# Kernel optimization log

Measured on AMD Instinct MI355X. Metric: run time of the kernel, lower is better.

Reference implementation:

```python
import jax, jax.numpy as jnp
import numpy as np

B, N = 32, 8192
NUM_CLASSES = 40
SA1_DIMS = (3, 64, 64, 128)      # grouped relative xyz only (in_channels=3 -> no extra features)
SA2_DIMS = (131, 128, 128, 256)  # 128 SA1 features + 3 relative xyz
LOC_DIMS = (256, 256, 512, 1024)
GLOB_DIMS = (1024, 512, 256)


def _fps(xyz, m):
    """Farthest point sampling. xyz: [B,N,3] -> indices [B,m] (first index is point 0)."""
    b, n, _ = xyz.shape
    big = jnp.asarray(1e10, xyz.dtype)

    def step(carry, _):
        dists, last = carry                                   # [B,N], [B]
        p = jnp.take_along_axis(xyz, last[:, None, None], axis=1)  # [B,1,3]
        d = jnp.sum((xyz - p) ** 2, axis=-1)                  # [B,N]
        dists = jnp.minimum(dists, d)
        nxt = jnp.argmax(dists, axis=-1).astype(jnp.int32)
        return (dists, nxt), nxt

    init = (jnp.full((b, n), big, xyz.dtype), jnp.zeros((b,), jnp.int32))
    _, rest = jax.lax.scan(step, init, None, length=m - 1)    # [m-1,B]
    return jnp.concatenate([jnp.zeros((b, 1), jnp.int32), rest.T], axis=1)


def _ball_query(xyz, new_xyz, radius, k):
    """First-k points within radius of each centroid, padded with the first hit (CUDA ball_query semantics)."""
    d2 = jnp.sum((new_xyz[:, :, None, :] - xyz[:, None, :, :]) ** 2, axis=-1)  # [B,M,N]
    valid = d2 < radius * radius
    n = xyz.shape[1]
    ar = jnp.arange(n, dtype=jnp.int32)
    order_key = jnp.where(valid, ar, ar + n)                  # valid points sort first, in index order
    _, idx = jax.lax.top_k(-order_key, k)                     # [B,M,K] first-k valid indices
    num_valid = jnp.sum(valid, axis=-1)                       # [B,M]
    idx = jnp.where(jnp.arange(k) < num_valid[..., None], idx, idx[..., :1])
    return idx.astype(jnp.int32)


_gather = jax.vmap(lambda p, i: p[i])  # p:[N,C], i:[M,K] -> [M,K,C], vmapped over batch


def _sa(xyz, feats, m, radius, k, ws, bs):
    """PointNetSAModule: FPS -> ball query -> group (relative xyz [+feat]) -> SharedMLP -> max over K."""
    cidx = _fps(xyz, m)
    new_xyz = jnp.take_along_axis(xyz, cidx[:, :, None], axis=1)   # [B,m,3]
    idx = _ball_query(xyz, new_xyz, radius, k)                     # [B,m,k]
    x = _gather(xyz, idx) - new_xyz[:, :, None, :]                 # [B,m,k,3]
    if feats is not None:
        x = jnp.concatenate([x, _gather(feats, idx)], axis=-1)
    for w, b in zip(ws, bs):  # Conv2d(1x1)+BN(eval, folded)+ReLU
        x = jax.nn.relu(jnp.einsum('bmkc,oc->bmko', x, w) + b)
    return new_xyz, jnp.max(x, axis=2)                             # [B,m,C_out]


def _forward(points, sa1_w0, sa1_b0, sa1_w1, sa1_b1, sa1_w2, sa1_b2,
             sa2_w0, sa2_b0, sa2_w1, sa2_b1, sa2_w2, sa2_b2,
             loc_w0, loc_b0, loc_w1, loc_b1, loc_w2, loc_b2,
             glob_w0, glob_b0, glob_w1, glob_b1, cls_w, cls_b):
    xyz = jnp.transpose(points, (0, 2, 1))                         # [B,N,3]
    new_xyz, feats = _sa(xyz, None, 512, 0.2, 32,
                         (sa1_w0, sa1_w1, sa1_w2), (sa1_b0, sa1_b1, sa1_b2))
    _, feats = _sa(new_xyz, feats, 128, 0.4, 64,
                   (sa2_w0, sa2_w1, sa2_w2), (sa2_b0, sa2_b1, sa2_b2))
    x = feats                                                      # [B,128,256]
    for w, b in ((loc_w0, loc_b0), (loc_w1, loc_b1), (loc_w2, loc_b2)):
        x = jax.nn.relu(jnp.einsum('bnc,oc->bno', x, w) + b)       # SharedMLP (Conv1d+BN+ReLU)
    x = jnp.max(x, axis=1)                                         # global max-pool -> [B,1024]
    for w, b in ((glob_w0, glob_b0), (glob_w1, glob_b1)):          # MLP (dropout in eval = identity)
        x = jax.nn.relu(x @ w.T + b)
    return x @ cls_w.T + cls_b                                     # cls_logits [B,40]


def setup_inputs() -> dict:
    key = jax.random.key(0)
    ks = iter(jax.random.split(key, 64))
    inp = {}
    # unit-cube point cloud so radii 0.2/0.4 are geometrically meaningful
    inp['points'] = jax.random.uniform(next(ks), (B, 3, N), jnp.float32, -1.0, 1.0)

    def lin(co, ci):
        return jax.random.normal(next(ks), (co, ci), jnp.float32) / np.sqrt(ci)

    for name, dims in (('sa1', SA1_DIMS), ('sa2', SA2_DIMS), ('loc', LOC_DIMS)):
        for i in range(len(dims) - 1):
            inp[f'{name}_w{i}'] = lin(dims[i + 1], dims[i])
            inp[f'{name}_b{i}'] = 0.01 * jax.random.normal(next(ks), (dims[i + 1],), jnp.float32)
    for i in range(2):
        inp[f'glob_w{i}'] = lin(GLOB_DIMS[i + 1], GLOB_DIMS[i])
        inp[f'glob_b{i}'] = 0.01 * jax.random.normal(next(ks), (GLOB_DIMS[i + 1],), jnp.float32)
    inp['cls_w'] = lin(NUM_CLASSES, GLOB_DIMS[-1])
    inp['cls_b'] = jnp.zeros((NUM_CLASSES,), jnp.float32)
    return inp


def reference(points, sa1_w0, sa1_b0, sa1_w1, sa1_b1, sa1_w2, sa1_b2,
              sa2_w0, sa2_b0, sa2_w1, sa2_b1, sa2_w2, sa2_b2,
              loc_w0, loc_b0, loc_w1, loc_b1, loc_w2, loc_b2,
              glob_w0, glob_b0, glob_w1, glob_b1, cls_w, cls_b):
    return _forward(points, sa1_w0, sa1_b0, sa1_w1, sa1_b1, sa1_w2, sa1_b2,
                    sa2_w0, sa2_b0, sa2_w1, sa2_b1, sa2_w2, sa2_b2,
                    loc_w0, loc_b0, loc_w1, loc_b1, loc_w2, loc_b2,
                    glob_w0, glob_b0, glob_w1, glob_b1, cls_w, cls_b)
```

## Files before the change

### kernel.cpp

```cpp
#include <hip/hip_runtime.h>
#include <hip/hip_bf16.h>
#include <cstdint>

#define CDIV(a,b) (((a)+(b)-1)/(b))

typedef short s8v __attribute__((ext_vector_type(8)));
typedef float f4v __attribute__((ext_vector_type(4)));
typedef float f2v __attribute__((ext_vector_type(2)));

__device__ __forceinline__ unsigned short f2bf_bits(float v) {
  __hip_bfloat16 b = __float2bfloat16(v);
  unsigned short u; __builtin_memcpy(&u, &b, 2);
  return u;
}
__device__ __forceinline__ void bsplit(float v, unsigned short& h, unsigned short& l) {
  __hip_bfloat16 hb = __float2bfloat16(v);
  float hf = __bfloat162float(hb);
  unsigned short hu; __builtin_memcpy(&hu, &hb, 2);
  h = hu;
  l = f2bf_bits(v - hf);
}

__device__ __forceinline__ void gl2lds16(const void* g, void* l, int lane) {
#if __has_builtin(__builtin_amdgcn_global_load_lds)
  __builtin_amdgcn_global_load_lds(
      (const __attribute__((address_space(1))) unsigned int*)g,
      (__attribute__((address_space(3))) unsigned int*)l, 16, 0, 0);
#else
  ((uint4*)l)[lane] = *(const uint4*)g;
#endif
}

__device__ __forceinline__ void agpr_put(float& slot, float v) {
  asm volatile("v_accvgpr_write_b32 %0, %1" : "=a"(slot) : "v"(v));
}
__device__ __forceinline__ float agpr_get(const float& slot) {
  float v;
  asm volatile("v_accvgpr_read_b32 %0, %1" : "=v"(v) : "a"(slot));
  return v;
}

__device__ __forceinline__ f2v pk_add(f2v a, f2v b) {
  f2v d; asm("v_pk_add_f32 %0, %1, %2" : "=v"(d) : "v"(a), "v"(b)); return d;
}
__device__ __forceinline__ f2v pk_mul(f2v a, f2v b) {
  f2v d; asm("v_pk_mul_f32 %0, %1, %2" : "=v"(d) : "v"(a), "v"(b)); return d;
}
__device__ __forceinline__ f2v pk_fma(f2v a, f2v b, f2v c) {
  f2v d; asm("v_pk_fma_f32 %0, %1, %2, %3" : "=v"(d) : "v"(a), "v"(b), "v"(c)); return d;
}

template<int C>
__device__ __forceinline__ unsigned dpp32(unsigned v) {
  return (unsigned)__builtin_amdgcn_update_dpp((int)v, (int)v, C, 0xF, 0xF, false);
}
template<int C>
__device__ __forceinline__ unsigned long long red_key(unsigned long long pk) {
  unsigned lo = dpp32<C>((unsigned)pk);
  unsigned hi = dpp32<C>((unsigned)(pk >> 32));
  unsigned long long p2 = ((unsigned long long)hi << 32) | lo;
  return (p2 > pk) ? p2 : pk;
}

template<int NPTS, int MOUT, int NTHR>
__global__ __launch_bounds__(NTHR, 1) void fps_kernel(
    const float* __restrict__ pts, int bstride, int cstride,
    int* __restrict__ out_idx)
{
  constexpr int PPT = NPTS / NTHR;
  constexpr int NP2 = PPT / 2;
  constexpr int NW  = NTHR / 64;
  const int b = blockIdx.x, t = threadIdx.x;
  const int lane = t & 63;
  const int wid = t >> 6;
  const float* px = pts + (size_t)b * bstride;
  const float* py = px + cstride;
  const float* pz = px + 2 * cstride;
  __shared__ float s_x[NPTS], s_y[NPTS], s_z[NPTS];
  __shared__ unsigned long long s_key[2][NW];
  __shared__ int s_out[MOUT];

  float ax[PPT], ay[PPT], az[PPT];
  f2v dsv[NP2];
#pragma unroll
  for (int j = 0; j < PPT; ++j) {
    int i = t + j * NTHR;
    float x = px[i], y = py[i], z = pz[i];
    s_x[i] = x; s_y[i] = y; s_z[i] = z;
    agpr_put(ax[j], x); agpr_put(ay[j], y); agpr_put(az[j], z);
  }
#pragma unroll
  for (int q = 0; q < NP2; ++q) dsv[q] = (f2v){1e10f, 1e10f};
  if (t == 0) s_out[0] = 0;
  float lx = px[0], ly = py[0], lz = pz[0];
  __syncthreads();

  for (int it = 1; it < MOUT; ++it) {
    const f2v nlx = (f2v){-lx, -lx};
    const f2v nly = (f2v){-ly, -ly};
    const f2v nlz = (f2v){-lz, -lz};
    float bestv = -1.0f; int bestj = 0;
#pragma unroll
    for (int q = 0; q < NP2; ++q) {
      f2v x2, y2, z2;
      x2.x = agpr_get(ax[2 * q]); x2.y = agpr_get(ax[2 * q + 1]);
      y2.x = agpr_get(ay[2 * q]); y2.y = agpr_get(ay[2 * q + 1]);
      z2.x = agpr_get(az[2 * q]); z2.y = agpr_get(az[2 * q + 1]);
      f2v dx = pk_add(x2, nlx);
      f2v dy = pk_add(y2, nly);
      f2v dz = pk_add(z2, nlz);
      f2v d2 = pk_fma(dz, dz, pk_fma(dy, dy, pk_mul(dx, dx)));
      float nd0 = fminf(dsv[q].x, d2.x);
      float nd1 = fminf(dsv[q].y, d2.y);
      dsv[q].x = nd0; dsv[q].y = nd1;
      if (nd0 > bestv) { bestv = nd0; bestj = 2 * q; }
      if (nd1 > bestv) { bestv = nd1; bestj = 2 * q + 1; }
    }
    const int besti = t + bestj * NTHR;
    unsigned long long pk =
        ((unsigned long long)__float_as_uint(bestv) << 32) | (unsigned)(~(unsigned)besti);
    pk = red_key<0x111>(pk);
    pk = red_key<0x112>(pk);
    pk = red_key<0x114>(pk);
    pk = red_key<0x118>(pk);
    pk = red_key<0x142>(pk);
    pk = red_key<0x143>(pk);
    int widx;
    if constexpr (NW == 1) {
      widx = (int)(~(unsigned)__builtin_amdgcn_readlane((int)(unsigned)pk, 63));
    } else {
      const int pb = it & 1;
      if (lane == 63) s_key[pb][wid] = pk;
      __syncthreads();
      unsigned long long ck = s_key[pb][lane & (NW - 1)];
      if (NW >= 2) ck = red_key<0x111>(ck);
      if (NW >= 4) ck = red_key<0x112>(ck);
      if (NW >= 8) ck = red_key<0x114>(ck);
      widx = (int)(~(unsigned)__builtin_amdgcn_readlane((int)(unsigned)ck, NW - 1));
    }
    lx = s_x[widx]; ly = s_y[widx]; lz = s_z[widx];
    if (t == 0) s_out[it] = widx;
  }
  __syncthreads();
  for (int i = t; i < MOUT; i += NTHR)
    out_idx[(size_t)b * MOUT + i] = s_out[i];
}

__global__ void gatherc_kernel(
    const float* __restrict__ pts, int bstride, int cstride,
    const int* __restrict__ cidx, int M,
    float* __restrict__ aos, float* __restrict__ soa)
{
  const int b = blockIdx.x, t = threadIdx.x;
  const int i = cidx[(size_t)b * M + t];
  const float* p = pts + (size_t)b * bstride;
  float x = p[i], y = p[cstride + i], z = p[2 * cstride + i];
  size_t g = (size_t)b * M + t;
  aos[g * 3 + 0] = x; aos[g * 3 + 1] = y; aos[g * 3 + 2] = z;
  soa[(size_t)b * 3 * M + t]         = x;
  soa[(size_t)b * 3 * M + M + t]     = y;
  soa[(size_t)b * 3 * M + 2 * M + t] = z;
}

template<int NPTS, int KNB, int MC>
__global__ __launch_bounds__(64) void ballq_wave(
    const float* __restrict__ pts, int bstride, int cstride,
    const float* __restrict__ cents, int* __restrict__ out, float r2)
{
  constexpr int NCH = NPTS / 64;
  const int g = blockIdx.x;
  const int b = g / MC;
  const int lane = threadIdx.x;
  const float* px = pts + (size_t)b * bstride;
  const float* py = px + cstride;
  const float* pz = px + 2 * cstride;
  const float cx = cents[g * 3 + 0], cy = cents[g * 3 + 1], cz = cents[g * 3 + 2];
  __shared__ int s_idx[KNB];
  float nx = px[lane], ny = py[lane], nz = pz[lane];
  int base = 0;
  for (int c = 0; c < NCH; ++c) {
    float X = nx, Y = ny, Z = nz;
    if (c + 1 < NCH) {
      int i2 = (c + 1) * 64 + lane;
      nx = px[i2]; ny = py[i2]; nz = pz[i2];
    }
    float dx = X - cx, dy = Y - cy, dz = Z - cz;
    bool valid = (dx * dx + dy * dy + dz * dz) < r2;
    unsigned long long mask = __ballot(valid);
    int rank = __popcll(mask & ((1ull << lane) - 1ull));
    int pos = base + rank;
    if (valid && pos < KNB) s_idx[pos] = c * 64 + lane;
    base += __popcll(mask);
    if (base >= KNB) break;
  }
  int total = base < KNB ? base : KNB;
  int first = s_idx[0];
  if (lane < KNB)
    out[(size_t)g * KNB + lane] = (lane < total) ? s_idx[lane] : first;
}

__global__ __launch_bounds__(256, 1) void sa1_fused(
    const float* __restrict__ pts, const int* __restrict__ idx1,
    const float* __restrict__ cents,
    const float* __restrict__ w0, const float* __restrict__ b0,
    const unsigned short* __restrict__ w1h, const unsigned short* __restrict__ w1l,
    const float* __restrict__ b1,
    const unsigned short* __restrict__ w2h, const unsigned short* __restrict__ w2l,
    const float* __restrict__ b2,
    unsigned short* __restrict__ f1h, unsigned short* __restrict__ f1l)
{
  __shared__ __align__(16) unsigned short sY[2][128 * 72];
  __shared__ __align__(16) unsigned short sZ[2][128 * 72];
  __shared__ __align__(16) unsigned short sW[2][64 * 72];
  __shared__ float sw0[192];
  __shared__ float sb0[64];

  const int tid = threadIdx.x, lane = tid & 63, wid = tid >> 6;
  const int wm = wid & 1, wn = wid >> 1;
  const int mn15 = lane & 15, kgrp = lane >> 4;
  const int bk = blockIdx.x;

  if (tid < 192) sw0[tid] = w0[tid];
  else sb0[tid - 192] = b0[tid - 192];
  for (int gi = tid; gi < 1024; gi += 256) {
    const int pl = gi >> 9, idx = gi & 511;
    const int n = idx >> 3, k8 = idx & 7;
    const uint4 v = ((const uint4*)(pl ? w1l : w1h))[idx];
    *(uint4*)&sW[pl][n * 72 + k8 * 8] = v;
  }
  __syncthreads();

  {
    const int rl = tid >> 1, half = tid & 1;
    const int r = bk * 128 + rl;
    const int gl = r >> 5, j = r & 31, b = gl >> 9;
    const int i = idx1[(size_t)gl * 32 + j];
    const float* px = pts + (size_t)b * 24576;
    const float x = px[i]         - cents[gl * 3 + 0];
    const float y = px[8192 + i]  - cents[gl * 3 + 1];
    const float z = px[16384 + i] - cents[gl * 3 + 2];
    union { unsigned short us[32]; uint4 v[4]; } ph, pl4;
#pragma unroll
    for (int u = 0; u < 32; ++u) {
      const int o = half * 32 + u;
      float v = sw0[o * 3] * x + sw0[o * 3 + 1] * y + sw0[o * 3 + 2] * z + sb0[o];
      v = fmaxf(v, 0.f);
      bsplit(v, ph.us[u], pl4.us[u]);
    }
    const int base = rl * 72 + half * 32;
#pragma unroll
    for (int g = 0; g < 4; ++g) {
      *(uint4*)&sY[0][base + g * 8] = ph.v[g];
      *(uint4*)&sY[1][base + g * 8] = pl4.v[g];
    }
  }
  __syncthreads();

  {
    f4v acc[4][2];
#pragma unroll
    for (int a = 0; a < 4; ++a)
#pragma unroll
      for (int c = 0; c < 2; ++c) acc[a][c] = (f4v){0.f, 0.f, 0.f, 0.f};
#pragma unroll
    for (int kc = 0; kc < 2; ++kc) {
      const int k0 = kc * 32;
      s8v af[2][4], bf[2][2];
#pragma unroll
      for (int mt = 0; mt < 4; ++mt) {
        const int m = wm * 64 + mt * 16 + mn15;
        af[0][mt] = *(const s8v*)&sY[0][m * 72 + k0 + kgrp * 8];
        af[1][mt] = *(const s8v*)&sY[1][m * 72 + k0 + kgrp * 8];
      }
#pragma unroll
      for (int nt = 0; nt < 2; ++nt) {
        const int n = wn * 32 + nt * 16 + mn15;
        bf[0][nt] = *(const s8v*)&sW[0][n * 72 + k0 + kgrp * 8];
        bf[1][nt] = *(const s8v*)&sW[1][n * 72 + k0 + kgrp * 8];
      }
#pragma unroll
      for (int mt = 0; mt < 4; ++mt)
#pragma unroll
        for (int nt = 0; nt < 2; ++nt) {
          acc[mt][nt] = __builtin_amdgcn_mfma_f32_16x16x32_bf16(af[0][mt], bf[0][nt], acc[mt][nt], 0, 0, 0);
          acc[mt][nt] = __builtin_amdgcn_mfma_f32_16x16x32_bf16(af[0][mt], bf[1][nt], acc[mt][nt], 0, 0, 0);
          acc[mt][nt] = __builtin_amdgcn_mfma_f32_16x16x32_bf16(af[1][mt], bf[0][nt], acc[mt][nt], 0, 0, 0);
        }
    }
#pragma unroll
    for (int nt = 0; nt < 2; ++nt) {
      const int n = wn * 32 + nt * 16 + mn15;
      const float bv = b1[n];
#pragma unroll
      for (int mt = 0; mt < 4; ++mt)
#pragma unroll
        for (int r = 0; r < 4; ++r) {
          const int m = wm * 64 + mt * 16 + (lane >> 4) * 4 + r;
          float v = fmaxf(acc[mt][nt][r] + bv, 0.f);
          unsigned short h, l; bsplit(v, h, l);
          sZ[0][m * 72 + n] = h;
          sZ[1][m * 72 + n] = l;
        }
    }
  }
  __syncthreads();

  for (int gi = tid; gi < 2048; gi += 256) {
    const int pl = gi >> 10, idx = gi & 1023;
    const int n = idx >> 3, k8 = idx & 7;
    const uint4 v = ((const uint4*)(pl ? w2l : w2h))[idx];
    *(uint4*)&sY[pl][n * 72 + k8 * 8] = v;
  }
  __syncthreads();

  {
    f4v acc[4][4];
#pragma unroll
    for (int a = 0; a < 4; ++a)
#pragma unroll
      for (int c = 0; c < 4; ++c) acc[a][c] = (f4v){0.f, 0.f, 0.f, 0.f};
#pragma unroll
    for (int kc = 0; kc < 2; ++kc) {
      const int k0 = kc * 32;
      s8v af[2][4], bf[2][4];
#pragma unroll
      for (int mt = 0; mt < 4; ++mt) {
        const int m = wm * 64 + mt * 16 + mn15;
        af[0][mt] = *(const s8v*)&sZ[0][m * 72 + k0 + kgrp * 8];
        af[1][mt] = *(const s8v*)&sZ[1][m * 72 + k0 + kgrp * 8];
      }
#pragma unroll
      for (int nt = 0; nt < 4; ++nt) {
        const int n = wn * 64 + nt * 16 + mn15;
        bf[0][nt] = *(const s8v*)&sY[0][n * 72 + k0 + kgrp * 8];
        bf[1][nt] = *(const s8v*)&sY[1][n * 72 + k0 + kgrp * 8];
      }
#pragma unroll
      for (int mt = 0; mt < 4; ++mt)
#pragma unroll
        for (int nt = 0; nt < 4; ++nt) {
          acc[mt][nt] = __builtin_amdgcn_mfma_f32_16x16x32_bf16(af[0][mt], bf[0][nt], acc[mt][nt], 0, 0, 0);
          acc[mt][nt] = __builtin_amdgcn_mfma_f32_16x16x32_bf16(af[0][mt], bf[1][nt], acc[mt][nt], 0, 0, 0);
          acc[mt][nt] = __builtin_amdgcn_mfma_f32_16x16x32_bf16(af[1][mt], bf[0][nt], acc[mt][nt], 0, 0, 0);
        }
    }
#pragma unroll
    for (int gq = 0; gq < 2; ++gq)
#pragma unroll
      for (int nt = 0; nt < 4; ++nt) {
        const int n = wn * 64 + nt * 16 + mn15;
        float v = -1e30f;
#pragma unroll
        for (int mt = 2 * gq; mt < 2 * gq + 2; ++mt)
#pragma unroll
          for (int r = 0; r < 4; ++r) v = fmaxf(v, acc[mt][nt][r]);
        v = fmaxf(v + b2[n], 0.f);
        v = fmaxf(v, __shfl_xor(v, 16, 64));
        v = fmaxf(v, __shfl_xor(v, 32, 64));
        if (lane < 16) {
          const size_t row = (size_t)bk * 4 + wm * 2 + gq;
          unsigned short h, l; bsplit(v, h, l);
          f1h[row * 128 + n] = h;
          f1l[row * 128 + n] = l;
        }
      }
  }
}

__global__ void gather2p_kernel(
    const float* __restrict__ nx1_aos,
    const unsigned short* __restrict__ f1h, const unsigned short* __restrict__ f1l,
    const int* __restrict__ idx2, const float* __restrict__ nx2_aos,
    unsigned short* __restrict__ Xh, unsigned short* __restrict__ Xl, int g0)
{
  const int r = blockIdx.x * 4 + threadIdx.y;
  const int lane = threadIdx.x;
  int gl = r >> 6, j = r & 63;
  int gg = g0 + gl;
  int b  = gg >> 7;
  int i  = idx2[(size_t)gg * 64 + j];
  int p  = b * 512 + i;
  size_t ro = (size_t)r * 160;
  const int slot = lane & 31;
  const bool isL = lane >= 32;
  unsigned short* dst = isL ? Xl : Xh;
  const unsigned short* f1 = isL ? f1l : f1h;
  if (slot < 16) {
    ((uint4*)(dst + ro))[slot] = ((const uint4*)(f1 + (size_t)p * 128))[slot];
  } else if (slot == 16) {
    union { unsigned short us[8]; uint4 v; } pk;
#pragma unroll
    for (int u = 0; u < 8; ++u) pk.us[u] = 0;
#pragma unroll
    for (int c = 0; c < 3; ++c) {
      float v = nx1_aos[(size_t)p * 3 + c] - nx2_aos[(size_t)gg * 3 + c];
      unsigned short h, l; bsplit(v, h, l);
      pk.us[c] = isL ? l : h;
    }
    ((uint4*)(dst + ro))[16] = pk.v;
  } else if (slot <= 19) {
    ((uint4*)(dst + ro))[slot] = make_uint4(0, 0, 0, 0);
  }
}

struct WSplitArgs {
  const float* src[9];
  unsigned short* h[9];
  unsigned short* l[9];
  int K[9];
  int KP[9];
  int perm[9];
  int cum[10];
};
__global__ void wsplit_all(WSplitArgs a) {
  int i = blockIdx.x * 256 + threadIdx.x;
  if (i >= a.cum[9]) return;
  int s = 0;
#pragma unroll
  for (int t = 1; t < 9; ++t) s += (i >= a.cum[t]);
  int local = i - a.cum[s];
  int KP = a.KP[s], K = a.K[s];
  int r = local / KP, k = local - r * KP;
  int oc;
  if (a.perm[s]) oc = (k < 128) ? k + 3 : (k < 131 ? k - 128 : -1);
  else           oc = (k < K) ? k : -1;
  float v = (oc >= 0) ? a.src[s][(size_t)r * K + oc] : 0.f;
  unsigned short hb, lb; bsplit(v, hb, lb);
  a.h[s][local] = hb; a.l[s][local] = lb;
}

template<int BN, int POOL>
__global__ __launch_bounds__(256, 1) void mfma_gemm(
    const unsigned short* __restrict__ Ah, const unsigned short* __restrict__ Al,
    const unsigned short* __restrict__ Wh, const unsigned short* __restrict__ Wl,
    const float* __restrict__ bias,
    unsigned short* __restrict__ Ch, unsigned short* __restrict__ Cl,
    float* __restrict__ Cf,
    unsigned short* __restrict__ Chp, unsigned short* __restrict__ Clp,
    int Kdim, int Ndim)
{
  constexpr int WTN = BN / 2, NT = WTN / 16;
  __shared__ unsigned short sA[2][128 * 32];
  __shared__ unsigned short sW[2][BN * 32];
  __shared__ float sPool[4][WTN];
  const int tid = threadIdx.x, lane = tid & 63, wid = tid >> 6;
  const int wm = wid & 1, wn = wid >> 1;
  const size_t bm0 = (size_t)blockIdx.y * 128;
  const int bn0 = blockIdx.x * BN;
  const int mn15 = lane & 15, kgrp = lane >> 4;

  f4v acc[4][NT];
#pragma unroll
  for (int a = 0; a < 4; ++a)
#pragma unroll
    for (int b = 0; b < NT; ++b) acc[a][b] = (f4v){0.f, 0.f, 0.f, 0.f};

  const int sc = lane & 3, srl = lane >> 2;

  for (int k0 = 0; k0 < Kdim; k0 += 32) {
#pragma unroll
    for (int hh = 0; hh < 2; ++hh) {
      const int R = wid * 32 + hh * 16;
      const int m = R + srl;
      const int kg = (sc - m - (m >> 2)) & 3;
      const size_t go = (bm0 + m) * (size_t)Kdim + k0 + kg * 8;
      gl2lds16(Ah + go, &sA[0][R * 32], lane);
      gl2lds16(Al + go, &sA[1][R * 32], lane);
    }
    if (BN == 128) {
#pragma unroll
      for (int hh = 0; hh < 2; ++hh) {
        const int R = wid * 32 + hh * 16;
        const int n = R + srl;
        const int kg = (sc - n - (n >> 2)) & 3;
        const size_t go = (size_t)(bn0 + n) * Kdim + k0 + kg * 8;
        gl2lds16(Wh + go, &sW[0][R * 32], lane);
        gl2lds16(Wl + go, &sW[1][R * 32], lane);
      }
    } else {
      const int R = wid * 16;
      const int n = R + srl;
      const int kg = (sc - n - (n >> 2)) & 3;
      const size_t go = (size_t)(bn0 + n) * Kdim + k0 + kg * 8;
      gl2lds16(Wh + go, &sW[0][R * 32], lane);
      gl2lds16(Wl + go, &sW[1][R * 32], lane);
    }
    __syncthreads();

    s8v af[2][4], bfr[2][NT];
#pragma unroll
    for (int mt = 0; mt < 4; ++mt) {
      const int m = wm * 64 + mt * 16 + mn15;
      const int cc = (kgrp + m + (m >> 2)) & 3;
      af[0][mt] = *(const s8v*)&sA[0][m * 32 + cc * 8];
      af[1][mt] = *(const s8v*)&sA[1][m * 32 + cc * 8];
    }
#pragma unroll
    for (int nt = 0; nt < NT; ++nt) {
      const int n = wn * WTN + nt * 16 + mn15;
      const int cc = (kgrp + n + (n >> 2)) & 3;
      bfr[0][nt] = *(const s8v*)&sW[0][n * 32 + cc * 8];
      bfr[1][nt] = *(const s8v*)&sW[1][n * 32 + cc * 8];
    }
#pragma unroll
    for (int mt = 0; mt < 4; ++mt)
#pragma unroll
      for (int nt = 0; nt < NT; ++nt) {
        acc[mt][nt] = __builtin_amdgcn_mfma_f32_16x16x32_bf16(af[0][mt], bfr[0][nt], acc[mt][nt], 0, 0, 0);
        acc[mt][nt] = __builtin_amdgcn_mfma_f32_16x16x32_bf16(af[0][mt], bfr[1][nt], acc[mt][nt], 0, 0, 0);
        acc[mt][nt] = __builtin_amdgcn_mfma_f32_16x16x32_bf16(af[1][mt], bfr[0][nt], acc[mt][nt], 0, 0, 0);
      }
    __syncthreads();
  }

  float bv[NT];
#pragma unroll
  for (int nt = 0; nt < NT; ++nt) bv[nt] = bias[bn0 + wn * WTN + nt * 16 + mn15];

  if (POOL == 0) {
#pragma unroll
    for (int mt = 0; mt < 4; ++mt)
#pragma unroll
      for (int nt = 0; nt < NT; ++nt) {
        const int n = bn0 + wn * WTN + nt * 16 + mn15;
#pragma unroll
        for (int r = 0; r < 4; ++r) {
          const size_t m = bm0 + wm * 64 + mt * 16 + (lane >> 4) * 4 + r;
          float v = fmaxf(acc[mt][nt][r] + bv[nt], 0.f);
          unsigned short h, l; bsplit(v, h, l);
          Ch[m * Ndim + n] = h;
          Cl[m * Ndim + n] = l;
        }
      }
  } else if (POOL == 32) {
#pragma unroll
    for (int gq = 0; gq < 2; ++gq)
#pragma unroll
      for (int nt = 0; nt < NT; ++nt) {
        float v = -1e30f;
#pragma unroll
        for (int mt = 2 * gq; mt < 2 * gq + 2; ++mt)
#pragma unroll
          for (int r = 0; r < 4; ++r) v = fmaxf(v, acc[mt][nt][r]);
        v = fmaxf(v + bv[nt], 0.f);
        v = fmaxf(v, __shfl_xor(v, 16, 64));
        v = fmaxf(v, __shfl_xor(v, 32, 64));
        if (lane < 16) {
          const int n = bn0 + wn * WTN + nt * 16 + mn15;
          const size_t row = bm0 / 32 + wm * 2 + gq;
          if (Chp) { unsigned short h, l; bsplit(v, h, l);
                     Chp[row * Ndim + n] = h; Clp[row * Ndim + n] = l; }
          if (Cf) Cf[row * Ndim + n] = v;
        }
      }
  } else if (POOL == 64) {
#pragma unroll
    for (int nt = 0; nt < NT; ++nt) {
      float v = -1e30f;
#pragma unroll
      for (int mt = 0; mt < 4; ++mt)
#pragma unroll
        for (int r = 0; r < 4; ++r) v = fmaxf(v, acc[mt][nt][r]);
      v = fmaxf(v + bv[nt], 0.f);
      v = fmaxf(v, __shfl_xor(v, 16, 64));
      v = fmaxf(v, __shfl_xor(v, 32, 64));
      if (lane < 16) {
        const int n = bn0 + wn * WTN + nt * 16 + mn15;
        const size_t row = bm0 / 64 + wm;
        if (Chp) { unsigned short h, l; bsplit(v, h, l);
                   Chp[row * Ndim + n] = h; Clp[row * Ndim + n] = l; }
        if (Cf) Cf[row * Ndim + n] = v;
      }
    }
  } else {
    float part[NT];
#pragma unroll
    for (int nt = 0; nt < NT; ++nt) {
      float v = -1e30f;
#pragma unroll
      for (int mt = 0; mt < 4; ++mt)
#pragma unroll
        for (int r = 0; r < 4; ++r) v = fmaxf(v, acc[mt][nt][r]);
      v = fmaxf(v + bv[nt], 0.f);
      v = fmaxf(v, __shfl_xor(v, 16, 64));
      v = fmaxf(v, __shfl_xor(v, 32, 64));
      part[nt] = v;
      if (lane < 16) sPool[wid][nt * 16 + mn15] = v;
    }
    __syncthreads();
    if (wm == 0 && lane < 16) {
#pragma unroll
      for (int nt = 0; nt < NT; ++nt) {
        float v = fmaxf(part[nt], sPool[wid + 1][nt * 16 + mn15]);
        const int n = bn0 + wn * WTN + nt * 16 + mn15;
        if (Cf) Cf[(size_t)(bm0 / 128) * Ndim + n] = v;
      }
    }
  }
}

__global__ __launch_bounds__(256) void head_kernel(
    const float* __restrict__ pooled,
    const float* __restrict__ w0, const float* __restrict__ b0,
    const float* __restrict__ w1, const float* __restrict__ b1,
    const float* __restrict__ wc, const float* __restrict__ bc,
    float* __restrict__ out)
{
  __shared__ float sx[1024];
  __shared__ float sy[512];
  __shared__ float sz[256];
  const int b = blockIdx.x, t = threadIdx.x;
  for (int i = t; i < 1024; i += 256) sx[i] = pooled[(size_t)b * 1024 + i];
  __syncthreads();
  for (int o = t; o < 512; o += 256) {
    const float4* w4 = (const float4*)(w0 + (size_t)o * 1024);
    const float4* x4 = (const float4*)sx;
    float acc = 0.f;
#pragma unroll 4
    for (int k = 0; k < 256; ++k) {
      float4 w = w4[k], x = x4[k];
      acc += w.x * x.x + w.y * x.y + w.z * x.z + w.w * x.w;
    }
    sy[o] = fmaxf(acc + b0[o], 0.f);
  }
  __syncthreads();
  if (t < 256) {
    const float4* w4 = (const float4*)(w1 + (size_t)t * 512);
    const float4* y4 = (const float4*)sy;
    float acc = 0.f;
#pragma unroll 4
    for (int k = 0; k < 128; ++k) {
      float4 w = w4[k], y = y4[k];
      acc += w.x * y.x + w.y * y.y + w.z * y.z + w.w * y.w;
    }
    sz[t] = fmaxf(acc + b1[t], 0.f);
  }
  __syncthreads();
  if (t < 40) {
    const float4* w4 = (const float4*)(wc + (size_t)t * 256);
    const float4* z4 = (const float4*)sz;
    float acc = 0.f;
#pragma unroll 4
    for (int k = 0; k < 64; ++k) {
      float4 w = w4[k], z = z4[k];
      acc += w.x * z.x + w.y * z.y + w.z * z.z + w.w * z.w;
    }
    out[(size_t)b * 40 + t] = acc + bc[t];
  }
}

extern "C" void kernel_launch(void* const* d_in, const int* in_sizes, int n_in,
                              void* d_out, int out_size, void* d_ws, size_t ws_size,
                              hipStream_t stream)
{
  (void)in_sizes; (void)n_in; (void)out_size; (void)ws_size;

  const float* points  = (const float*)d_in[0];
  const float* sa1_w[3] = {(const float*)d_in[1], (const float*)d_in[3], (const float*)d_in[5]};
  const float* sa1_b[3] = {(const float*)d_in[2], (const float*)d_in[4], (const float*)d_in[6]};
  const float* sa2_w[3] = {(const float*)d_in[7], (const float*)d_in[9], (const float*)d_in[11]};
  const float* sa2_b[3] = {(const float*)d_in[8], (const float*)d_in[10], (const float*)d_in[12]};
  const float* loc_w[3] = {(const float*)d_in[13], (const float*)d_in[15], (const float*)d_in[17]};
  const float* loc_b[3] = {(const float*)d_in[14], (const float*)d_in[16], (const float*)d_in[18]};
  const float* glob_w0 = (const float*)d_in[19];
  const float* glob_b0 = (const float*)d_in[20];
  const float* glob_w1 = (const float*)d_in[21];
  const float* glob_b1 = (const float*)d_in[22];
  const float* cls_w   = (const float*)d_in[23];
  const float* cls_b   = (const float*)d_in[24];

  char* base = (char*)d_ws;
  size_t off = 0;
  auto alloc = [&](size_t nbytes) -> void* {
    void* p = base + off;
    off += (nbytes + 255) & ~(size_t)255;
    return p;
  };

  const size_t XE = (size_t)65536 * 160;
  const size_t YE = (size_t)131072 * 64;
  unsigned short* Xh = (unsigned short*)alloc(XE * 2);
  unsigned short* Xl = (unsigned short*)alloc(XE * 2);
  unsigned short* Yh = (unsigned short*)alloc(YE * 2);
  unsigned short* Yl = (unsigned short*)alloc(YE * 2);
  unsigned short* f1h = (unsigned short*)alloc((size_t)16384 * 128 * 2);
  unsigned short* f1l = (unsigned short*)alloc((size_t)16384 * 128 * 2);
  unsigned short* f2h = (unsigned short*)alloc((size_t)4096 * 256 * 2);
  unsigned short* f2l = (unsigned short*)alloc((size_t)4096 * 256 * 2);

  const int  wrows[9] = {64, 64, 128, 128, 128, 256, 256, 512, 1024};
  const int  wK[9]    = {3, 64, 64, 131, 128, 128, 256, 256, 512};
  const int  wKP[9]   = {32, 64, 64, 160, 128, 128, 256, 256, 512};
  const float* wsrc[9] = {sa1_w[0], sa1_w[1], sa1_w[2],
                          sa2_w[0], sa2_w[1], sa2_w[2],
                          loc_w[0], loc_w[1], loc_w[2]};
  unsigned short *wph[9], *wpl[9];
  WSplitArgs wa;
  int cum = 0;
  for (int s = 0; s < 9; ++s) {
    size_t e = (size_t)wrows[s] * wKP[s];
    wph[s] = (unsigned short*)alloc(e * 2);
    wpl[s] = (unsigned short*)alloc(e * 2);
    wa.src[s] = wsrc[s]; wa.h[s] = wph[s]; wa.l[s] = wpl[s];
    wa.K[s] = wK[s]; wa.KP[s] = wKP[s]; wa.cum[s] = cum;
    wa.perm[s] = (s == 3) ? 1 : 0;
    cum += wrows[s] * wKP[s];
  }
  wa.cum[9] = cum;

  float* nx1_aos = (float*)alloc((size_t)32 * 512 * 3 * 4);
  float* nx1_soa = (float*)alloc((size_t)32 * 512 * 3 * 4);
  int*   cidx1   = (int*)  alloc((size_t)32 * 512 * 4);
  int*   idx1    = (int*)  alloc((size_t)32 * 512 * 32 * 4);
  float* nx2_aos = (float*)alloc((size_t)32 * 128 * 3 * 4);
  float* nx2_soa = (float*)alloc((size_t)32 * 128 * 3 * 4);
  int*   cidx2   = (int*)  alloc((size_t)32 * 128 * 4);
  int*   idx2    = (int*)  alloc((size_t)32 * 128 * 64 * 4);
  float* pooled  = (float*)alloc((size_t)32 * 1024 * 4);

  const float r2a = (float)(0.2 * 0.2);
  const float r2b = (float)(0.4 * 0.4);

  wsplit_all<<<CDIV(cum, 256), 256, 0, stream>>>(wa);

  fps_kernel<8192, 512, 512><<<32, 512, 0, stream>>>(points, 24576, 8192, cidx1);
  gatherc_kernel<<<32, 512, 0, stream>>>(points, 24576, 8192, cidx1, 512, nx1_aos, nx1_soa);
  ballq_wave<8192, 32, 512><<<32 * 512, 64, 0, stream>>>(points, 24576, 8192, nx1_aos, idx1, r2a);

  sa1_fused<<<4096, 256, 0, stream>>>(
      points, idx1, nx1_aos, sa1_w[0], sa1_b[0],
      wph[1], wpl[1], sa1_b[1], wph[2], wpl[2], sa1_b[2], f1h, f1l);

  fps_kernel<512, 128, 64><<<32, 64, 0, stream>>>(nx1_soa, 1536, 512, cidx2);
  gatherc_kernel<<<32, 128, 0, stream>>>(nx1_soa, 1536, 512, cidx2, 128, nx2_aos, nx2_soa);
  ballq_wave<512, 64, 128><<<32 * 128, 64, 0, stream>>>(nx1_soa, 1536, 512, nx2_aos, idx2, r2b);

  for (int c = 0; c < 4; ++c) {
    const int g0 = c * 1024;
    const int rows = 1024 * 64;
    gather2p_kernel<<<dim3(rows / 4), dim3(64, 4), 0, stream>>>(
        nx1_aos, f1h, f1l, idx2, nx2_aos, Xh, Xl, g0);
    mfma_gemm<128, 0><<<dim3(1, rows / 128), 256, 0, stream>>>(
        Xh, Xl, wph[3], wpl[3], sa2_b[0], Yh, Yl, nullptr, nullptr, nullptr, 160, 128);
    mfma_gemm<128, 0><<<dim3(1, rows / 128), 256, 0, stream>>>(
        Yh, Yl, wph[4], wpl[4], sa2_b[1], Xh, Xl, nullptr, nullptr, nullptr, 128, 128);
    mfma_gemm<128, 64><<<dim3(2, rows / 128), 256, 0, stream>>>(
        Xh, Xl, wph[5], wpl[5], sa2_b[2], nullptr, nullptr, nullptr,
        f2h + (size_t)g0 * 256, f2l + (size_t)g0 * 256, 128, 256);
  }

  mfma_gemm<128, 0><<<dim3(2, 32), 256, 0, stream>>>(
      f2h, f2l, wph[6], wpl[6], loc_b[0], Yh, Yl, nullptr, nullptr, nullptr, 256, 256);
  mfma_gemm<128, 0><<<dim3(4, 32), 256, 0, stream>>>(
      Yh, Yl, wph[7], wpl[7], loc_b[1], Xh, Xl, nullptr, nullptr, nullptr, 256, 512);
  mfma_gemm<128, 128><<<dim3(8, 32), 256, 0, stream>>>(
      Xh, Xl, wph[8], wpl[8], loc_b[2], nullptr, nullptr, pooled, nullptr, nullptr, 512, 1024);

  head_kernel<<<32, 256, 0, stream>>>(pooled, glob_w0, glob_b0,
                                      glob_w1, glob_b1, cls_w, cls_b, (float*)d_out);
}
```

Measured before the change: 1.286 ms.

## Fuse SA2 gather and three-layer MLP with max-pool into one kernel

Replaces the chunked SA2 pipeline (gather kernel plus three separate GEMM launches per chunk, with intermediates written to global memory) with a single kernel per group. Each block gathers its 64 neighbour rows into LDS, runs the three split-bf16 MFMA layers keeping activations in shared memory, and max-pools straight into the f2 output. This removes the large global round-trips of intermediate activations and the extra launches. In exchange, weights are streamed per block from global/L2 with small per-wave tiles, and the large LDS footprint with launch_bounds(256,1) may limit occupancy.

```diff
diff --git a/kernel.cpp b/kernel.cpp
--- a/kernel.cpp
+++ b/kernel.cpp
@@ -367,39 +367,250 @@
   }
 }
 
-__global__ void gather2p_kernel(
-    const float* __restrict__ nx1_aos,
+__global__ __launch_bounds__(256, 1) void sa2_fused(
     const unsigned short* __restrict__ f1h, const unsigned short* __restrict__ f1l,
-    const int* __restrict__ idx2, const float* __restrict__ nx2_aos,
-    unsigned short* __restrict__ Xh, unsigned short* __restrict__ Xl, int g0)
+    const float* __restrict__ nx1_aos, const float* __restrict__ nx2_aos,
+    const int* __restrict__ idx2,
+    const unsigned short* __restrict__ w1h, const unsigned short* __restrict__ w1l,
+    const float* __restrict__ b1,
+    const unsigned short* __restrict__ w2h, const unsigned short* __restrict__ w2l,
+    const float* __restrict__ b2,
+    const unsigned short* __restrict__ w3h, const unsigned short* __restrict__ w3l,
+    const float* __restrict__ b3,
+    unsigned short* __restrict__ f2h, unsigned short* __restrict__ f2l)
 {
-  const int r = blockIdx.x * 4 + threadIdx.y;
-  const int lane = threadIdx.x;
-  int gl = r >> 6, j = r & 63;
-  int gg = g0 + gl;
-  int b  = gg >> 7;
-  int i  = idx2[(size_t)gg * 64 + j];
-  int p  = b * 512 + i;
-  size_t ro = (size_t)r * 160;
-  const int slot = lane & 31;
-  const bool isL = lane >= 32;
-  unsigned short* dst = isL ? Xl : Xh;
-  const unsigned short* f1 = isL ? f1l : f1h;
-  if (slot < 16) {
-    ((uint4*)(dst + ro))[slot] = ((const uint4*)(f1 + (size_t)p * 128))[slot];
-  } else if (slot == 16) {
-    union { unsigned short us[8]; uint4 v; } pk;
-#pragma unroll
-    for (int u = 0; u < 8; ++u) pk.us[u] = 0;
-#pragma unroll
-    for (int c = 0; c < 3; ++c) {
-      float v = nx1_aos[(size_t)p * 3 + c] - nx2_aos[(size_t)gg * 3 + c];
-      unsigned short h, l; bsplit(v, h, l);
-      pk.us[c] = isL ? l : h;
-    }
-    ((uint4*)(dst + ro))[16] = pk.v;
-  } else if (slot <= 19) {
-    ((uint4*)(dst + ro))[slot] = make_uint4(0, 0, 0, 0);
+  __shared__ __align__(16) unsigned short sX[2][64 * 160];
+  __shared__ __align__(16) unsigned short sY[2][64 * 136];
+  __shared__ __align__(16) unsigned short sW[4][2][32 * 40];
+
+  const int tid = threadIdx.x, lane = tid & 63, wid = tid >> 6;
+  const int mn15 = lane & 15, kgrp = lane >> 4;
+  const int gg = blockIdx.x;
+  const int bb = gg >> 7;
+
+  {
+    const int r = tid >> 2, q = tid & 3;
+    const int i = idx2[(size_t)gg * 64 + r];
+    const int p = bb * 512 + i;
+#pragma unroll
+    for (int pl = 0; pl < 2; ++pl) {
+      const uint4* src = (const uint4*)((pl ? f1l : f1h) + (size_t)p * 128);
+#pragma unroll
+      for (int g = 0; g < 4; ++g)
+        *(uint4*)&sX[pl][r * 160 + (q * 4 + g) * 8] = src[q * 4 + g];
+    }
+    if (q == 0) {
+      union { unsigned short us[8]; uint4 v; } ph, pl4;
+#pragma unroll
+      for (int u = 0; u < 8; ++u) { ph.us[u] = 0; pl4.us[u] = 0; }
+#pragma unroll
+      for (int c = 0; c < 3; ++c) {
+        float v = nx1_aos[(size_t)p * 3 + c] - nx2_aos[(size_t)gg * 3 + c];
+        bsplit(v, ph.us[c], pl4.us[c]);
+      }
+      *(uint4*)&sX[0][r * 160 + 128] = ph.v;
+      *(uint4*)&sX[1][r * 160 + 128] = pl4.v;
+    } else {
+      uint4 z = make_uint4(0, 0, 0, 0);
+      *(uint4*)&sX[0][r * 160 + 128 + q * 8] = z;
+      *(uint4*)&sX[1][r * 160 + 128 + q * 8] = z;
+    }
+  }
+  __syncthreads();
+
+  const int spl = lane >> 5, srow = lane & 31;
+  unsigned short* swb = &sW[wid][0][0];
+
+  {
+    f4v acc[4][2];
+#pragma unroll
+    for (int a = 0; a < 4; ++a)
+#pragma unroll
+      for (int c = 0; c < 2; ++c) acc[a][c] = (f4v){0.f, 0.f, 0.f, 0.f};
+    uint4 pf[4];
+    {
+      const unsigned short* s = (spl ? w1l : w1h) + (size_t)(wid * 32 + srow) * 160;
+#pragma unroll
+      for (int g = 0; g < 4; ++g) pf[g] = *(const uint4*)(s + g * 8);
+    }
+#pragma unroll
+    for (int c = 0; c < 5; ++c) {
+      unsigned short* d = swb + spl * 1280 + srow * 40;
+#pragma unroll
+      for (int g = 0; g < 4; ++g) *(uint4*)(d + g * 8) = pf[g];
+      if (c < 4) {
+        const unsigned short* s = (spl ? w1l : w1h) + (size_t)(wid * 32 + srow) * 160 + (c + 1) * 32;
+#pragma unroll
+        for (int g = 0; g < 4; ++g) pf[g] = *(const uint4*)(s + g * 8);
+      }
+      const int k0 = c * 32;
+      s8v af[2][4], bf[2][2];
+#pragma unroll
+      for (int mt = 0; mt < 4; ++mt) {
+        const int m = mt * 16 + mn15;
+        af[0][mt] = *(const s8v*)&sX[0][m * 160 + k0 + kgrp * 8];
+        af[1][mt] = *(const s8v*)&sX[1][m * 160 + k0 + kgrp * 8];
+      }
+#pragma unroll
+      for (int nt = 0; nt < 2; ++nt) {
+        const int nl = nt * 16 + mn15;
+        bf[0][nt] = *(const s8v*)&swb[0 * 1280 + nl * 40 + kgrp * 8];
+        bf[1][nt] = *(const s8v*)&swb[1 * 1280 + nl * 40 + kgrp * 8];
+      }
+#pragma unroll
+      for (int mt = 0; mt < 4; ++mt)
+#pragma unroll
+        for (int nt = 0; nt < 2; ++nt) {
+          acc[mt][nt] = __builtin_amdgcn_mfma_f32_16x16x32_bf16(af[0][mt], bf[0][nt], acc[mt][nt], 0, 0, 0);
+          acc[mt][nt] = __builtin_amdgcn_mfma_f32_16x16x32_bf16(af[0][mt], bf[1][nt], acc[mt][nt], 0, 0, 0);
+          acc[mt][nt] = __builtin_amdgcn_mfma_f32_16x16x32_bf16(af[1][mt], bf[0][nt], acc[mt][nt], 0, 0, 0);
+        }
+    }
+#pragma unroll
+    for (int nt = 0; nt < 2; ++nt) {
+      const int n = wid * 32 + nt * 16 + mn15;
+      const float bv = b1[n];
+#pragma unroll
+      for (int mt = 0; mt < 4; ++mt)
+#pragma unroll
+        for (int r = 0; r < 4; ++r) {
+          const int m = mt * 16 + kgrp * 4 + r;
+          float v = fmaxf(acc[mt][nt][r] + bv, 0.f);
+          unsigned short h, l; bsplit(v, h, l);
+          sY[0][m * 136 + n] = h;
+          sY[1][m * 136 + n] = l;
+        }
+    }
+  }
+  __syncthreads();
+
+  {
+    f4v acc[4][2];
+#pragma unroll
+    for (int a = 0; a < 4; ++a)
+#pragma unroll
+      for (int c = 0; c < 2; ++c) acc[a][c] = (f4v){0.f, 0.f, 0.f, 0.f};
+    uint4 pf[4];
+    {
+      const unsigned short* s = (spl ? w2l : w2h) + (size_t)(wid * 32 + srow) * 128;
+#pragma unroll
+      for (int g = 0; g < 4; ++g) pf[g] = *(const uint4*)(s + g * 8);
+    }
+#pragma unroll
+    for (int c = 0; c < 4; ++c) {
+      unsigned short* d = swb + spl * 1280 + srow * 40;
+#pragma unroll
+      for (int g = 0; g < 4; ++g) *(uint4*)(d + g * 8) = pf[g];
+      if (c < 3) {
+        const unsigned short* s = (spl ? w2l : w2h) + (size_t)(wid * 32 + srow) * 128 + (c + 1) * 32;
+#pragma unroll
+        for (int g = 0; g < 4; ++g) pf[g] = *(const uint4*)(s + g * 8);
+      }
+      const int k0 = c * 32;
+      s8v af[2][4], bf[2][2];
+#pragma unroll
+      for (int mt = 0; mt < 4; ++mt) {
+        const int m = mt * 16 + mn15;
+        af[0][mt] = *(const s8v*)&sY[0][m * 136 + k0 + kgrp * 8];
+        af[1][mt] = *(const s8v*)&sY[1][m * 136 + k0 + kgrp * 8];
+      }
+#pragma unroll
+      for (int nt = 0; nt < 2; ++nt) {
+        const int nl = nt * 16 + mn15;
+        bf[0][nt] = *(const s8v*)&swb[0 * 1280 + nl * 40 + kgrp * 8];
+        bf[1][nt] = *(const s8v*)&swb[1 * 1280 + nl * 40 + kgrp * 8];
+      }
+#pragma unroll
+      for (int mt = 0; mt < 4; ++mt)
+#pragma unroll
+        for (int nt = 0; nt < 2; ++nt) {
+          acc[mt][nt] = __builtin_amdgcn_mfma_f32_16x16x32_bf16(af[0][mt], bf[0][nt], acc[mt][nt], 0, 0, 0);
+          acc[mt][nt] = __builtin_amdgcn_mfma_f32_16x16x32_bf16(af[0][mt], bf[1][nt], acc[mt][nt], 0, 0, 0);
+          acc[mt][nt] = __builtin_amdgcn_mfma_f32_16x16x32_bf16(af[1][mt], bf[0][nt], acc[mt][nt], 0, 0, 0);
+        }
+    }
+#pragma unroll
+    for (int nt = 0; nt < 2; ++nt) {
+      const int n = wid * 32 + nt * 16 + mn15;
+      const float bv = b2[n];
+#pragma unroll
+      for (int mt = 0; mt < 4; ++mt)
+#pragma unroll
+        for (int r = 0; r < 4; ++r) {
+          const int m = mt * 16 + kgrp * 4 + r;
+          float v = fmaxf(acc[mt][nt][r] + bv, 0.f);
+          unsigned short h, l; bsplit(v, h, l);
+          sX[0][m * 136 + n] = h;
+          sX[1][m * 136 + n] = l;
+        }
+    }
+  }
+  __syncthreads();
+
+#pragma unroll
+  for (int h = 0; h < 2; ++h) {
+    f4v acc[4][2];
+#pragma unroll
+    for (int a = 0; a < 4; ++a)
+#pragma unroll
+      for (int c = 0; c < 2; ++c) acc[a][c] = (f4v){0.f, 0.f, 0.f, 0.f};
+    const int nb = wid * 64 + h * 32;
+    uint4 pf[4];
+    {
+      const unsigned short* s = (spl ? w3l : w3h) + (size_t)(nb + srow) * 128;
+#pragma unroll
+      for (int g = 0; g < 4; ++g) pf[g] = *(const uint4*)(s + g * 8);
+    }
+#pragma unroll
+    for (int c = 0; c < 4; ++c) {
+      unsigned short* d = swb + spl * 1280 + srow * 40;
+#pragma unroll
+      for (int g = 0; g < 4; ++g) *(uint4*)(d + g * 8) = pf[g];
+      if (c < 3) {
+        const unsigned short* s = (spl ? w3l : w3h) + (size_t)(nb + srow) * 128 + (c + 1) * 32;
+#pragma unroll
+        for (int g = 0; g < 4; ++g) pf[g] = *(const uint4*)(s + g * 8);
+      }
+      const int k0 = c * 32;
+      s8v af[2][4], bf[2][2];
+#pragma unroll
+      for (int mt = 0; mt < 4; ++mt) {
+        const int m = mt * 16 + mn15;
+        af[0][mt] = *(const s8v*)&sX[0][m * 136 + k0 + kgrp * 8];
+        af[1][mt] = *(const s8v*)&sX[1][m * 136 + k0 + kgrp * 8];
+      }
+#pragma unroll
+      for (int nt = 0; nt < 2; ++nt) {
+        const int nl = nt * 16 + mn15;
+        bf[0][nt] = *(const s8v*)&swb[0 * 1280 + nl * 40 + kgrp * 8];
+        bf[1][nt] = *(const s8v*)&swb[1 * 1280 + nl * 40 + kgrp * 8];
+      }
+#pragma unroll
+      for (int mt = 0; mt < 4; ++mt)
+#pragma unroll
+        for (int nt = 0; nt < 2; ++nt) {
+          acc[mt][nt] = __builtin_amdgcn_mfma_f32_16x16x32_bf16(af[0][mt], bf[0][nt], acc[mt][nt], 0, 0, 0);
+          acc[mt][nt] = __builtin_amdgcn_mfma_f32_16x16x32_bf16(af[0][mt], bf[1][nt], acc[mt][nt], 0, 0, 0);
+          acc[mt][nt] = __builtin_amdgcn_mfma_f32_16x16x32_bf16(af[1][mt], bf[0][nt], acc[mt][nt], 0, 0, 0);
+        }
+    }
+#pragma unroll
+    for (int nt = 0; nt < 2; ++nt) {
+      const int n = nb + nt * 16 + mn15;
+      float v = -1e30f;
+#pragma unroll
+      for (int mt = 0; mt < 4; ++mt)
+#pragma unroll
+        for (int r = 0; r < 4; ++r) v = fmaxf(v, acc[mt][nt][r]);
+      v = fmaxf(v + b3[n], 0.f);
+      v = fmaxf(v, __shfl_xor(v, 16, 64));
+      v = fmaxf(v, __shfl_xor(v, 32, 64));
+      if (lane < 16) {
+        unsigned short hh, ll; bsplit(v, hh, ll);
+        f2h[(size_t)gg * 256 + n] = hh;
+        f2l[(size_t)gg * 256 + n] = ll;
+      }
+    }
   }
 }
 
@@ -532,46 +743,6 @@
           Cl[m * Ndim + n] = l;
         }
       }
-  } else if (POOL == 32) {
-#pragma unroll
-    for (int gq = 0; gq < 2; ++gq)
-#pragma unroll
-      for (int nt = 0; nt < NT; ++nt) {
-        float v = -1e30f;
-#pragma unroll
-        for (int mt = 2 * gq; mt < 2 * gq + 2; ++mt)
-#pragma unroll
-          for (int r = 0; r < 4; ++r) v = fmaxf(v, acc[mt][nt][r]);
-        v = fmaxf(v + bv[nt], 0.f);
-        v = fmaxf(v, __shfl_xor(v, 16, 64));
-        v = fmaxf(v, __shfl_xor(v, 32, 64));
-        if (lane < 16) {
-          const int n = bn0 + wn * WTN + nt * 16 + mn15;
-          const size_t row = bm0 / 32 + wm * 2 + gq;
-          if (Chp) { unsigned short h, l; bsplit(v, h, l);
-                     Chp[row * Ndim + n] = h; Clp[row * Ndim + n] = l; }
-          if (Cf) Cf[row * Ndim + n] = v;
-        }
-      }
-  } else if (POOL == 64) {
-#pragma unroll
-    for (int nt = 0; nt < NT; ++nt) {
-      float v = -1e30f;
-#pragma unroll
-      for (int mt = 0; mt < 4; ++mt)
-#pragma unroll
-        for (int r = 0; r < 4; ++r) v = fmaxf(v, acc[mt][nt][r]);
-      v = fmaxf(v + bv[nt], 0.f);
-      v = fmaxf(v, __shfl_xor(v, 16, 64));
-      v = fmaxf(v, __shfl_xor(v, 32, 64));
-      if (lane < 16) {
-        const int n = bn0 + wn * WTN + nt * 16 + mn15;
-        const size_t row = bm0 / 64 + wm;
-        if (Chp) { unsigned short h, l; bsplit(v, h, l);
-                   Chp[row * Ndim + n] = h; Clp[row * Ndim + n] = l; }
-        if (Cf) Cf[row * Ndim + n] = v;
-      }
-    }
   } else {
     float part[NT];
 #pragma unroll
@@ -677,8 +848,8 @@
     return p;
   };
 
-  const size_t XE = (size_t)65536 * 160;
-  const size_t YE = (size_t)131072 * 64;
+  const size_t XE = (size_t)4096 * 512;
+  const size_t YE = (size_t)4096 * 256;
   unsigned short* Xh = (unsigned short*)alloc(XE * 2);
   unsigned short* Xl = (unsigned short*)alloc(XE * 2);
   unsigned short* Yh = (unsigned short*)alloc(YE * 2);
@@ -735,19 +906,12 @@
   gatherc_kernel<<<32, 128, 0, stream>>>(nx1_soa, 1536, 512, cidx2, 128, nx2_aos, nx2_soa);
   ballq_wave<512, 64, 128><<<32 * 128, 64, 0, stream>>>(nx1_soa, 1536, 512, nx2_aos, idx2, r2b);
 
-  for (int c = 0; c < 4; ++c) {
-    const int g0 = c * 1024;
-    const int rows = 1024 * 64;
-    gather2p_kernel<<<dim3(rows / 4), dim3(64, 4), 0, stream>>>(
-        nx1_aos, f1h, f1l, idx2, nx2_aos, Xh, Xl, g0);
-    mfma_gemm<128, 0><<<dim3(1, rows / 128), 256, 0, stream>>>(
-        Xh, Xl, wph[3], wpl[3], sa2_b[0], Yh, Yl, nullptr, nullptr, nullptr, 160, 128);
-    mfma_gemm<128, 0><<<dim3(1, rows / 128), 256, 0, stream>>>(
-        Yh, Yl, wph[4], wpl[4], sa2_b[1], Xh, Xl, nullptr, nullptr, nullptr, 128, 128);
-    mfma_gemm<128, 64><<<dim3(2, rows / 128), 256, 0, stream>>>(
-        Xh, Xl, wph[5], wpl[5], sa2_b[2], nullptr, nullptr, nullptr,
-        f2h + (size_t)g0 * 256, f2l + (size_t)g0 * 256, 128, 256);
-  }
+  sa2_fused<<<4096, 256, 0, stream>>>(
+      f1h, f1l, nx1_aos, nx2_aos, idx2,
+      wph[3], wpl[3], sa2_b[0],
+      wph[4], wpl[4], sa2_b[1],
+      wph[5], wpl[5], sa2_b[2],
+      f2h, f2l);
 
   mfma_gemm<128, 0><<<dim3(2, 32), 256, 0, stream>>>(
       f2h, f2l, wph[6], wpl[6], loc_b[0], Yh, Yl, nullptr, nullptr, nullptr, 256, 256);
```

Result: faster. 1.197 ms (-6.9%).
